# Kernel optimization log

Hardware: AMD Instinct MI355X
Metric: run time of the kernel (lower is better)

Reference implementation:

```python
import jax, jax.numpy as jnp
import numpy as np

NUM_GAUSSIANS = 20
NUM_LETTERS = 80
HIDDEN_SIZE = 400
ATTENTION_SCALE = 0.05
B, U = 1024, 1024


def setup_inputs() -> dict:
    key = jax.random.key(0)
    k1, k2, k3, k4, k5 = jax.random.split(key, 5)
    text_inputs = jax.random.randint(k1, (B, U), 0, NUM_LETTERS)          # [B, U] int
    text_lengths = jax.random.randint(k2, (B,), 0, U)                     # [B] int
    y_0 = jax.random.normal(k3, (B, HIDDEN_SIZE), dtype=jnp.float32)      # [B, H]
    prev_k = jax.random.uniform(k4, (B, NUM_GAUSSIANS), dtype=jnp.float32)  # [B, N]
    # window_layer params: Linear(H, 3N)
    kw, kb = jax.random.split(k5)
    lim = 1.0 / np.sqrt(HIDDEN_SIZE)
    W = jax.random.uniform(kw, (3 * NUM_GAUSSIANS, HIDDEN_SIZE), minval=-lim, maxval=lim, dtype=jnp.float32)
    bias = jax.random.uniform(kb, (3 * NUM_GAUSSIANS,), minval=-lim, maxval=lim, dtype=jnp.float32)
    return {"text_inputs": text_inputs, "text_lengths": text_lengths,
            "y_0": y_0, "prev_k": prev_k, "W": W, "bias": bias}


def reference(text_inputs, text_lengths, y_0, prev_k, W, bias):
    N = prev_k.shape[1]
    batch, maxlen = text_inputs.shape
    out = y_0 @ W.T + bias                                   # [B, 3N]
    a = jnp.exp(out[:, :N])[..., None]                       # [B, N, 1]
    b = jnp.exp(out[:, N:2 * N])[..., None]                  # [B, N, 1]
    k = (jnp.exp(out[:, 2 * N:]) * ATTENTION_SCALE + prev_k)[..., None]  # [B, N, 1]
    u = jnp.arange(maxlen, dtype=out.dtype)[None, None, :]   # [1, 1, U]
    text_mask = (jnp.arange(maxlen)[None, :] < text_lengths[:, None]).astype(out.dtype)  # [B, U]
    phi_t_u = jnp.sum(a * jnp.exp(-b * (k - u) ** 2), axis=1) * text_mask  # [B, U]
    # w_t = sum_u one_hot(text)[b,u,:] * phi[b,u]  ==  scatter-add over letter dim
    rows = jnp.arange(batch)[:, None]                        # [B, 1]
    w_t = jnp.zeros((batch, NUM_LETTERS), dtype=out.dtype).at[rows, text_inputs].add(phi_t_u)  # [B, L]
    return (w_t, k[..., 0], phi_t_u)
```

## Files before the change

kernel.cpp:

```cpp
#include <hip/hip_runtime.h>

#define NG 20
#define NL 80
#define HS 400
#define ASCALE 0.05f
#define BB 1024
#define UU 1024
#define LOG2E 1.4426950408889634f

__global__ __launch_bounds__(256, 4) void window_fused_kernel(
    const int*   __restrict__ text,
    const int*   __restrict__ tlen,
    const float* __restrict__ y0,
    const float* __restrict__ prevk,
    const float* __restrict__ W,
    const float* __restrict__ bias,
    float* __restrict__ w_t,
    float* __restrict__ k_out,
    float* __restrict__ phi_out)
{
    const int b   = blockIdx.x;
    const int tid = threadIdx.x;

    const int4 letters = reinterpret_cast<const int4*>(text + b * UU)[tid];
    const int  len     = tlen[b];

    __shared__ __align__(16) float4 p4s[NG];
    __shared__ float wloc[NL];
    __shared__ float umax_s;

    if (tid < NL) wloc[tid] = 0.f;

    if (tid < 3 * NG * 4) {
        const int j = tid >> 2;
        const int p = tid & 3;
        const float4* wr = reinterpret_cast<const float4*>(W + j * HS + p * 100);
        const float4* yr = reinterpret_cast<const float4*>(y0 + b * HS + p * 100);
        float s = 0.f;
        #pragma unroll 5
        for (int i = 0; i < 25; ++i) {
            const float4 w4 = wr[i];
            const float4 y4 = yr[i];
            s += w4.x * y4.x + w4.y * y4.y + w4.z * y4.z + w4.w * y4.w;
        }
        s += __shfl_down(s, 1, 4);
        s += __shfl_down(s, 2, 4);
        if (p == 0) {
            const float val = s + bias[j];
            if (j < NG) {
                p4s[j].x = val * LOG2E;
            } else if (j < 2 * NG) {
                p4s[j - NG].y = __expf(val) * LOG2E;
            } else {
                const int g = j - 2 * NG;
                const float kk = __expf(val) * ASCALE + prevk[b * NG + g];
                p4s[g].z = kk;
                k_out[b * NG + g] = kk;
            }
        }
    }
    __syncthreads();

    if (tid < 32) {
        float reach = -1.f;
        if (tid < NG) {
            const float4 g = p4s[tid];
            const float num = fmaxf(g.x + 60.f, 0.f);
            reach = g.z + __builtin_sqrtf(num / g.y);
        }
        #pragma unroll
        for (int off = 16; off; off >>= 1)
            reach = fmaxf(reach, __shfl_down(reach, off, 32));
        if (tid == 0) umax_s = reach;
    }
    __syncthreads();

    const float umax = umax_s;
    const int u0 = tid * 4;
    float s0 = 0.f, s1 = 0.f, s2 = 0.f, s3 = 0.f;
    if (u0 < len && (float)u0 <= umax) {
        const float uf = (float)u0;
        #pragma unroll
        for (int n = 0; n < NG; ++n) {
            const float4 g = p4s[n];
            const float d0 = g.z - uf;
            const float d1 = d0 - 1.f;
            const float d2 = d0 - 2.f;
            const float d3 = d0 - 3.f;
            s0 += __builtin_amdgcn_exp2f(__builtin_fmaf(-g.y * d0, d0, g.x));
            s1 += __builtin_amdgcn_exp2f(__builtin_fmaf(-g.y * d1, d1, g.x));
            s2 += __builtin_amdgcn_exp2f(__builtin_fmaf(-g.y * d2, d2, g.x));
            s3 += __builtin_amdgcn_exp2f(__builtin_fmaf(-g.y * d3, d3, g.x));
        }
        if (u0 + 1 >= len) s1 = 0.f;
        if (u0 + 2 >= len) s2 = 0.f;
        if (u0 + 3 >= len) s3 = 0.f;
    }
    float4 phi4; phi4.x = s0; phi4.y = s1; phi4.z = s2; phi4.w = s3;
    reinterpret_cast<float4*>(phi_out + b * UU)[tid] = phi4;

    if (s0 != 0.f) atomicAdd(&wloc[letters.x], s0);
    if (s1 != 0.f) atomicAdd(&wloc[letters.y], s1);
    if (s2 != 0.f) atomicAdd(&wloc[letters.z], s2);
    if (s3 != 0.f) atomicAdd(&wloc[letters.w], s3);
    __syncthreads();

    if (tid < NL) w_t[b * NL + tid] = wloc[tid];
}

extern "C" void kernel_launch(void* const* d_in, const int* in_sizes, int n_in,
                              void* d_out, int out_size, void* d_ws, size_t ws_size,
                              hipStream_t stream) {
    const int*   text  = (const int*)  d_in[0];
    const int*   tlen  = (const int*)  d_in[1];
    const float* y0    = (const float*)d_in[2];
    const float* prevk = (const float*)d_in[3];
    const float* W     = (const float*)d_in[4];
    const float* bias  = (const float*)d_in[5];

    float* out   = (float*)d_out;
    float* w_t   = out;
    float* k_out = out + BB * NL;
    float* phi   = out + BB * NL + BB * NG;

    hipLaunchKernelGGL(window_fused_kernel, dim3(BB), dim3(256), 0, stream,
                       text, tlen, y0, prevk, W, bias, w_t, k_out, phi);
}
```

Before: 81.76 us.

## Process four batch rows per block to reuse W weights from registers

Each block now handles four batch rows. It stages their y0 rows in shared memory and keeps its slice of W in registers, reusing it across the rows. The Gaussian evaluation and scatter-add loop over the rows sequentially. This cuts redundant W loads and the block count by four, at the cost of fewer blocks in flight and more registers per thread.

New measurement: 76.22 us. 1.07x faster.

```diff
diff --git a/kernel.cpp b/kernel.cpp
--- a/kernel.cpp
+++ b/kernel.cpp
@@ -7,8 +7,9 @@
 #define BB 1024
 #define UU 1024
 #define LOG2E 1.4426950408889634f
+#define ROWS 4
 
-__global__ __launch_bounds__(256, 4) void window_fused_kernel(
+__global__ __launch_bounds__(256) void window_fused4(
     const int*   __restrict__ text,
     const int*   __restrict__ tlen,
     const float* __restrict__ y0,
@@ -19,93 +20,122 @@
     float* __restrict__ k_out,
     float* __restrict__ phi_out)
 {
-    const int b   = blockIdx.x;
+    const int b0  = blockIdx.x * ROWS;
     const int tid = threadIdx.x;
 
-    const int4 letters = reinterpret_cast<const int4*>(text + b * UU)[tid];
-    const int  len     = tlen[b];
+    int4 letters[ROWS];
+    int  len[ROWS];
+    #pragma unroll
+    for (int r = 0; r < ROWS; ++r) {
+        letters[r] = reinterpret_cast<const int4*>(text + (b0 + r) * UU)[tid];
+        len[r]     = tlen[b0 + r];
+    }
 
-    __shared__ __align__(16) float4 p4s[NG];
-    __shared__ float wloc[NL];
-    __shared__ float umax_s;
+    __shared__ __align__(16) float  yrow[ROWS][HS];
+    __shared__ __align__(16) float4 p4s[ROWS][NG];
+    __shared__ float wloc[ROWS][NL];
+    __shared__ float umax_s[ROWS];
 
-    if (tid < NL) wloc[tid] = 0.f;
+    for (int i = tid; i < ROWS * HS / 4; i += 256) {
+        reinterpret_cast<float4*>(&yrow[0][0])[i] =
+            reinterpret_cast<const float4*>(y0 + b0 * HS)[i];
+    }
+    for (int i = tid; i < ROWS * NL; i += 256) (&wloc[0][0])[i] = 0.f;
+    __syncthreads();
 
     if (tid < 3 * NG * 4) {
         const int j = tid >> 2;
         const int p = tid & 3;
+        float4 wreg[25];
         const float4* wr = reinterpret_cast<const float4*>(W + j * HS + p * 100);
-        const float4* yr = reinterpret_cast<const float4*>(y0 + b * HS + p * 100);
-        float s = 0.f;
-        #pragma unroll 5
-        for (int i = 0; i < 25; ++i) {
-            const float4 w4 = wr[i];
-            const float4 y4 = yr[i];
-            s += w4.x * y4.x + w4.y * y4.y + w4.z * y4.z + w4.w * y4.w;
-        }
-        s += __shfl_down(s, 1, 4);
-        s += __shfl_down(s, 2, 4);
-        if (p == 0) {
-            const float val = s + bias[j];
-            if (j < NG) {
-                p4s[j].x = val * LOG2E;
-            } else if (j < 2 * NG) {
-                p4s[j - NG].y = __expf(val) * LOG2E;
-            } else {
-                const int g = j - 2 * NG;
-                const float kk = __expf(val) * ASCALE + prevk[b * NG + g];
-                p4s[g].z = kk;
-                k_out[b * NG + g] = kk;
+        #pragma unroll
+        for (int i = 0; i < 25; ++i) wreg[i] = wr[i];
+        const float bj = bias[j];
+
+        #pragma unroll
+        for (int r = 0; r < ROWS; ++r) {
+            const float4* yr = reinterpret_cast<const float4*>(&yrow[r][p * 100]);
+            float sa = 0.f, sb = 0.f;
+            #pragma unroll
+            for (int i = 0; i < 25; ++i) {
+                const float4 w4 = wreg[i];
+                const float4 y4 = yr[i];
+                sa += w4.x * y4.x + w4.y * y4.y;
+                sb += w4.z * y4.z + w4.w * y4.w;
+            }
+            float s = sa + sb;
+            s += __shfl_down(s, 1, 4);
+            s += __shfl_down(s, 2, 4);
+            if (p == 0) {
+                const int row = b0 + r;
+                const float val = s + bj;
+                if (j < NG) {
+                    p4s[r][j].x = val * LOG2E;
+                } else if (j < 2 * NG) {
+                    p4s[r][j - NG].y = __expf(val) * LOG2E;
+                } else {
+                    const int g = j - 2 * NG;
+                    const float kk = __expf(val) * ASCALE + prevk[row * NG + g];
+                    p4s[r][g].z = kk;
+                    k_out[row * NG + g] = kk;
+                }
             }
         }
     }
     __syncthreads();
 
-    if (tid < 32) {
+    if (tid < ROWS * 32) {
+        const int r = tid >> 5;
+        const int n = tid & 31;
         float reach = -1.f;
-        if (tid < NG) {
-            const float4 g = p4s[tid];
-            const float num = fmaxf(g.x + 60.f, 0.f);
-            reach = g.z + __builtin_sqrtf(num / g.y);
+        if (n < NG) {
+            const float4 g = p4s[r][n];
+            reach = g.z + __builtin_sqrtf(fmaxf(g.x + 60.f, 0.f) / g.y);
         }
         #pragma unroll
         for (int off = 16; off; off >>= 1)
             reach = fmaxf(reach, __shfl_down(reach, off, 32));
-        if (tid == 0) umax_s = reach;
+        if (n == 0) umax_s[r] = reach;
     }
     __syncthreads();
 
-    const float umax = umax_s;
     const int u0 = tid * 4;
-    float s0 = 0.f, s1 = 0.f, s2 = 0.f, s3 = 0.f;
-    if (u0 < len && (float)u0 <= umax) {
-        const float uf = (float)u0;
-        #pragma unroll
-        for (int n = 0; n < NG; ++n) {
-            const float4 g = p4s[n];
-            const float d0 = g.z - uf;
-            const float d1 = d0 - 1.f;
-            const float d2 = d0 - 2.f;
-            const float d3 = d0 - 3.f;
-            s0 += __builtin_amdgcn_exp2f(__builtin_fmaf(-g.y * d0, d0, g.x));
-            s1 += __builtin_amdgcn_exp2f(__builtin_fmaf(-g.y * d1, d1, g.x));
-            s2 += __builtin_amdgcn_exp2f(__builtin_fmaf(-g.y * d2, d2, g.x));
-            s3 += __builtin_amdgcn_exp2f(__builtin_fmaf(-g.y * d3, d3, g.x));
+    const float uf = (float)u0;
+    #pragma unroll
+    for (int r = 0; r < ROWS; ++r) {
+        float s0 = 0.f, s1 = 0.f, s2 = 0.f, s3 = 0.f;
+        if (u0 < len[r] && uf <= umax_s[r]) {
+            #pragma unroll
+            for (int n = 0; n < NG; ++n) {
+                const float4 g = p4s[r][n];
+                const float d0 = g.z - uf;
+                const float d1 = d0 - 1.f;
+                const float d2 = d0 - 2.f;
+                const float d3 = d0 - 3.f;
+                s0 += __builtin_amdgcn_exp2f(__builtin_fmaf(-g.y * d0, d0, g.x));
+                s1 += __builtin_amdgcn_exp2f(__builtin_fmaf(-g.y * d1, d1, g.x));
+                s2 += __builtin_amdgcn_exp2f(__builtin_fmaf(-g.y * d2, d2, g.x));
+                s3 += __builtin_amdgcn_exp2f(__builtin_fmaf(-g.y * d3, d3, g.x));
+            }
+            if (u0 + 1 >= len[r]) s1 = 0.f;
+            if (u0 + 2 >= len[r]) s2 = 0.f;
+            if (u0 + 3 >= len[r]) s3 = 0.f;
         }
-        if (u0 + 1 >= len) s1 = 0.f;
-        if (u0 + 2 >= len) s2 = 0.f;
-        if (u0 + 3 >= len) s3 = 0.f;
+        float4 phi4; phi4.x = s0; phi4.y = s1; phi4.z = s2; phi4.w = s3;
+        reinterpret_cast<float4*>(phi_out + (b0 + r) * UU)[tid] = phi4;
+
+        if (s0 != 0.f) atomicAdd(&wloc[r][letters[r].x], s0);
+        if (s1 != 0.f) atomicAdd(&wloc[r][letters[r].y], s1);
+        if (s2 != 0.f) atomicAdd(&wloc[r][letters[r].z], s2);
+        if (s3 != 0.f) atomicAdd(&wloc[r][letters[r].w], s3);
     }
-    float4 phi4; phi4.x = s0; phi4.y = s1; phi4.z = s2; phi4.w = s3;
-    reinterpret_cast<float4*>(phi_out + b * UU)[tid] = phi4;
-
-    if (s0 != 0.f) atomicAdd(&wloc[letters.x], s0);
-    if (s1 != 0.f) atomicAdd(&wloc[letters.y], s1);
-    if (s2 != 0.f) atomicAdd(&wloc[letters.z], s2);
-    if (s3 != 0.f) atomicAdd(&wloc[letters.w], s3);
     __syncthreads();
 
-    if (tid < NL) w_t[b * NL + tid] = wloc[tid];
+    if (tid < NL) {
+        #pragma unroll
+        for (int r = 0; r < ROWS; ++r)
+            w_t[(b0 + r) * NL + tid] = wloc[r][tid];
+    }
 }
 
 extern "C" void kernel_launch(void* const* d_in, const int* in_sizes, int n_in,
@@ -123,6 +153,6 @@
     float* k_out = out + BB * NL;
     float* phi   = out + BB * NL + BB * NG;
 
-    hipLaunchKernelGGL(window_fused_kernel, dim3(BB), dim3(256), 0, stream,
+    hipLaunchKernelGGL(window_fused4, dim3(BB / ROWS), dim3(256), 0, stream,
                        text, tlen, y0, prevk, W, bias, w_t, k_out, phi);
 }
```
